# Kernel optimization log

Hardware: AMD Instinct MI355X
Metric: run time of the kernel (lower is better)

## Reference

```python
import jax, jax.numpy as jnp
import numpy as np

B, IN, OUT, P, NS = 256, 1024, 512, 1000, 128

def setup_inputs() -> dict:
    key = jax.random.key(0)
    ks = jax.random.split(key, 6)
    return {
        "x": jax.random.normal(ks[0], (B, IN), jnp.float32),
        "noise": jax.random.normal(ks[1], (B, NS, P), jnp.float32),
        "fb_w": jax.random.normal(ks[2], (1, IN), jnp.float32) * (1.0 / np.sqrt(IN)),
        "fb_b": jnp.zeros((1,), jnp.float32),
        "decay_param": jnp.full((1,), 0.1, jnp.float32),
        "conv_w": jax.random.normal(ks[3], (P, P, 3), jnp.float32) * (1.0 / np.sqrt(3 * P)),
        "conv_b": jnp.zeros((P,), jnp.float32),
        "out_w": jax.random.normal(ks[4], (OUT, P), jnp.float32) * (1.0 / np.sqrt(P)),
        "out_b": jnp.zeros((OUT,), jnp.float32),
    }


def reference(x, noise, fb_w, fb_b, decay_param, conv_w, conv_b, out_w, out_b):
    # x: [B, IN]; noise: [B, NS, P] (Brownian increments for the SDE kernel)
    n_steps = noise.shape[1]
    dt = 1.0 / n_steps                       # T = 1.0
    sd = jnp.sqrt(jnp.asarray(dt, x.dtype))
    # per-sample feedback value: sigmoid(feedback_controller(x))
    feedback = jax.nn.sigmoid(x @ fb_w.T + fb_b)            # [B, 1]
    # decay value: sigmoid(decay_controller) * 0.5 (scalar)
    decay = jax.nn.sigmoid(decay_param[0]) * 0.5
    retain = 1.0 - decay * dt
    # Batched Euler-Maruyama Brownian SDE: X_{t+1} = (1 - decay*dt) X_t + feedback*sqrt(dt)*eps_t
    eps = jnp.transpose(noise, (1, 0, 2))                    # [NS, B, P]
    x0 = jnp.zeros((x.shape[0], noise.shape[2]), x.dtype)

    def step(X, e):
        Xn = X * retain + feedback * sd * e
        return Xn, Xn

    _, paths = jax.lax.scan(step, x0, eps)                   # [NS, B, P]
    paths_bct = jnp.transpose(paths, (1, 2, 0))              # [B, P, NS]
    # temporal_aggregator: Conv1d(P, P, kernel=3, padding=1) over time, then mean over time
    agg = jax.lax.conv_general_dilated(
        paths_bct, conv_w, window_strides=(1,), padding=[(1, 1)],
        dimension_numbers=("NCH", "OIH", "NCH"))
    agg = (agg + conv_b[None, :, None]).mean(axis=2)         # [B, P]
    # output_projection: P -> OUT
    return agg @ out_w.T + out_b
```

## Files before the change

kernel.cpp:

```cpp
#include <hip/hip_runtime.h>
#include <hip/hip_bf16.h>

#define B_N   256
#define IN_N  1024
#define OUT_N 512
#define P_N   1000
#define NS_N  128

#define K1P   3072
#define N1P   1024
#define K2P   1024
#define SK1   16
#define SK2   8

typedef __attribute__((ext_vector_type(8))) short short8v;
typedef __attribute__((ext_vector_type(4))) float f32x4;
typedef unsigned short ushort_t;
typedef __attribute__((ext_vector_type(4))) unsigned short ushort4v;

__device__ __forceinline__ float sigmoid_f(float z) { return 1.0f / (1.0f + __expf(-z)); }

__device__ __forceinline__ ushort_t f2bf(float x) {
    return __bfloat16_as_ushort(__float2bfloat16(x));
}
__device__ __forceinline__ float bf2f(ushort_t h) {
    union { unsigned u; float f; } v; v.u = ((unsigned)h) << 16;
    return v.f;
}

__global__ __launch_bounds__(512) void sde_fused_kernel(const float* __restrict__ x,
                                                        const float* __restrict__ fb_w,
                                                        const float* __restrict__ fb_b,
                                                        const float* __restrict__ noise,
                                                        const float* __restrict__ decay_param,
                                                        ushort_t* __restrict__ Thi) {
    const int b  = blockIdx.x;
    const int ch = blockIdx.y;
    const int t  = threadIdx.x;
    const int cg = t & 127;
    const int tq = t >> 7;

    float2 xv = ((const float2*)(x + (size_t)b * IN_N))[t];
    float2 wv = ((const float2*)fb_w)[t];
    __shared__ float red[512];
    red[t] = xv.x * wv.x + xv.y * wv.y;
    __syncthreads();
    for (int off = 256; off >= 1; off >>= 1) {
        if (t < off) red[t] += red[t + off];
        __syncthreads();
    }
    float fbv = sigmoid_f(red[0] + fb_b[0]);

    float decay = sigmoid_f(decay_param[0]) * 0.5f;
    const float dt = 1.0f / NS_N;
    float retain = 1.0f - decay * dt;
    float inv_omr = 1.0f / (decay * dt);
    float r2 = retain * retain, r4 = r2 * r2, r8 = r4 * r4;
    float r16 = r8 * r8, r32 = r16 * r16;
    float r64 = r32 * r32, r96 = r64 * r32;

    const int c0 = ch * 512 + cg * 4;
    const bool act = (c0 < P_N);
    const float* base = noise + (size_t)b * NS_N * P_N + (act ? c0 : 0);

    float4 sE = {0, 0, 0, 0}, L = {0, 0, 0, 0};
    if (act) {
        const int s0 = tq * 32;
        float rp = 1.0f;
        #pragma unroll 8
        for (int ss = s0 + 31; ss >= s0; --ss) {
            float4 e = *(const float4*)(base + (size_t)ss * P_N);
            sE.x += e.x; sE.y += e.y; sE.z += e.z; sE.w += e.w;
            L.x += rp * e.x; L.y += rp * e.y; L.z += rp * e.z; L.w += rp * e.w;
            rp *= retain;
        }
    }

    __shared__ float4 xSE[3][128], xL[3][128], xF[128];
    if (tq < 3) { xSE[tq][cg] = sE; xL[tq][cg] = L; }
    if (tq == 0 && act) xF[cg] = *(const float4*)base;
    __syncthreads();

    if (tq == 3) {
        size_t tb = (size_t)b * K1P + 3 * (size_t)c0;
        if (!act) {
            #pragma unroll
            for (int j = 0; j < 12; ++j) Thi[tb + j] = 0;
            return;
        }
        float4 se0 = xSE[0][cg], se1 = xSE[1][cg], se2 = xSE[2][cg];
        float4 l0 = xL[0][cg], l1 = xL[1][cg], l2 = xL[2][cg], ff = xF[cg];
        float Se[4] = {se0.x + se1.x + se2.x + sE.x, se0.y + se1.y + se2.y + sE.y,
                       se0.z + se1.z + se2.z + sE.z, se0.w + se1.w + se2.w + sE.w};
        float Lv[4] = {L.x + r32 * l2.x + r64 * l1.x + r96 * l0.x,
                       L.y + r32 * l2.y + r64 * l1.y + r96 * l0.y,
                       L.z + r32 * l2.z + r64 * l1.z + r96 * l0.z,
                       L.w + r32 * l2.w + r64 * l1.w + r96 * l0.w};
        float Fv[4] = {ff.x, ff.y, ff.z, ff.w};
        float sd = sqrtf(dt);
        float scale = fbv * sd * (1.0f / NS_N);
        #pragma unroll
        for (int j = 0; j < 4; ++j) {
            float Aj = (Se[j] - retain * Lv[j]) * inv_omr;
            Thi[tb + 3 * j + 0] = f2bf(scale * (Aj - Lv[j]));
            Thi[tb + 3 * j + 1] = f2bf(scale * Aj);
            Thi[tb + 3 * j + 2] = f2bf(scale * (Aj - Fv[j]));
        }
    }
}

__global__ __launch_bounds__(512) void gemm_bf16_bm256(const ushort_t* __restrict__ A,
                                                       const float* __restrict__ B,
                                                       ushort_t* __restrict__ Cpart,
                                                       int lda, int ldb,
                                                       int Nvalid, int Kvalid,
                                                       int Kper, int ldc) {
    __shared__ __align__(16) ushort_t As[256 * 64];
    __shared__ __align__(16) ushort_t Bs[128 * 64];

    const int tid  = threadIdx.x;
    const int lane = tid & 63;
    const int wave = tid >> 6;
    const int r15  = lane & 15;
    const int g4   = lane >> 4;
    const int wrow = wave >> 1;
    const int wcol = wave & 1;
    const int n0 = blockIdx.x * 128;
    const size_t kbeg = (size_t)blockIdx.z * Kper;

    f32x4 acc[4][4] = {};

    for (int kt = 0; kt < Kper; kt += 64) {
        const size_t kk0 = kbeg + kt;
        #pragma unroll
        for (int c = 0; c < 4; ++c) {
            int chunk = tid + c * 512;
            int row = chunk >> 3;
            int g   = chunk & 7;
            int ldsoff = row * 64 + ((g ^ (row & 7)) << 3);
            *(short8v*)&As[ldsoff] = *(const short8v*)(A + (size_t)row * lda + kk0 + g * 8);
        }
        #pragma unroll
        for (int c = 0; c < 2; ++c) {
            int chunk = tid + c * 512;
            int row = chunk >> 3;
            int g   = chunk & 7;
            int ldsoff = row * 64 + ((g ^ (row & 7)) << 3);
            int k = (int)kk0 + g * 8;
            short8v bh = {0, 0, 0, 0, 0, 0, 0, 0};
            if ((n0 + row) < Nvalid && k < Kvalid) {
                const float* bp = B + (size_t)(n0 + row) * ldb + k;
                float4 b0 = *(const float4*)bp;
                float4 b1 = *(const float4*)(bp + 4);
                bh[0] = (short)f2bf(b0.x); bh[1] = (short)f2bf(b0.y);
                bh[2] = (short)f2bf(b0.z); bh[3] = (short)f2bf(b0.w);
                bh[4] = (short)f2bf(b1.x); bh[5] = (short)f2bf(b1.y);
                bh[6] = (short)f2bf(b1.z); bh[7] = (short)f2bf(b1.w);
            }
            *(short8v*)&Bs[ldsoff] = bh;
        }
        __syncthreads();

        #pragma unroll
        for (int ks = 0; ks < 2; ++ks) {
            const int g = ks * 4 + g4;
            short8v af[4], bf_[4];
            #pragma unroll
            for (int f = 0; f < 4; ++f) {
                int arow = wrow * 64 + f * 16 + r15;
                af[f] = *(const short8v*)&As[arow * 64 + ((g ^ (arow & 7)) << 3)];
            }
            #pragma unroll
            for (int f = 0; f < 4; ++f) {
                int brow = wcol * 64 + f * 16 + r15;
                bf_[f] = *(const short8v*)&Bs[brow * 64 + ((g ^ (brow & 7)) << 3)];
            }
            #pragma unroll
            for (int mf = 0; mf < 4; ++mf) {
                #pragma unroll
                for (int nf = 0; nf < 4; ++nf) {
                    acc[mf][nf] = __builtin_amdgcn_mfma_f32_16x16x32_bf16(af[mf], bf_[nf], acc[mf][nf], 0, 0, 0);
                }
            }
        }
        __syncthreads();
    }

    ushort_t* cp = Cpart + (size_t)blockIdx.z * B_N * ldc;
    #pragma unroll
    for (int mf = 0; mf < 4; ++mf) {
        #pragma unroll
        for (int nf = 0; nf < 4; ++nf) {
            #pragma unroll
            for (int r = 0; r < 4; ++r) {
                int m = wrow * 64 + mf * 16 + g4 * 4 + r;
                int n = n0 + wcol * 64 + nf * 16 + r15;
                cp[(size_t)m * ldc + n] = f2bf(acc[mf][nf][r]);
            }
        }
    }
}

__global__ __launch_bounds__(256) void reduce_agg_kernel(const ushort_t* __restrict__ Cpart1,
                                                         const float* __restrict__ conv_b,
                                                         ushort_t* __restrict__ agg) {
    int idx4 = (blockIdx.x * 256 + threadIdx.x) * 4;
    int n = idx4 & (N1P - 1);
    float s0 = 0.f, s1 = 0.f, s2 = 0.f, s3 = 0.f;
    if (n < P_N) {
        float4 cb = *(const float4*)(conv_b + n);
        s0 = cb.x; s1 = cb.y; s2 = cb.z; s3 = cb.w;
        #pragma unroll
        for (int z = 0; z < SK1; ++z) {
            ushort4v p = *(const ushort4v*)(Cpart1 + (size_t)z * (B_N * N1P) + idx4);
            s0 += bf2f(p[0]); s1 += bf2f(p[1]); s2 += bf2f(p[2]); s3 += bf2f(p[3]);
        }
    }
    ushort4v o = {f2bf(s0), f2bf(s1), f2bf(s2), f2bf(s3)};
    *(ushort4v*)(agg + idx4) = o;
}

__global__ __launch_bounds__(256) void reduce_out_kernel(const ushort_t* __restrict__ Cpart2,
                                                         const float* __restrict__ out_b,
                                                         float* __restrict__ out) {
    int idx4 = (blockIdx.x * 256 + threadIdx.x) * 4;
    int n = idx4 & (OUT_N - 1);
    float4 ob = *(const float4*)(out_b + n);
    float s0 = ob.x, s1 = ob.y, s2 = ob.z, s3 = ob.w;
    #pragma unroll
    for (int z = 0; z < SK2; ++z) {
        ushort4v p = *(const ushort4v*)(Cpart2 + (size_t)z * (B_N * OUT_N) + idx4);
        s0 += bf2f(p[0]); s1 += bf2f(p[1]); s2 += bf2f(p[2]); s3 += bf2f(p[3]);
    }
    float4 o = {s0, s1, s2, s3};
    *(float4*)(out + idx4) = o;
}

extern "C" void kernel_launch(void* const* d_in, const int* in_sizes, int n_in,
                              void* d_out, int out_size, void* d_ws, size_t ws_size,
                              hipStream_t stream) {
    const float* x           = (const float*)d_in[0];
    const float* noise       = (const float*)d_in[1];
    const float* fb_w        = (const float*)d_in[2];
    const float* fb_b        = (const float*)d_in[3];
    const float* decay_param = (const float*)d_in[4];
    const float* conv_w      = (const float*)d_in[5];
    const float* conv_b      = (const float*)d_in[6];
    const float* out_w       = (const float*)d_in[7];
    const float* out_b       = (const float*)d_in[8];
    float* out = (float*)d_out;

    char* ws = (char*)d_ws;
    size_t off = 0;
    ushort_t* Thi    = (ushort_t*)(ws + off); off += (size_t)B_N * K1P * 2;
    ushort_t* agg    = (ushort_t*)(ws + off); off += (size_t)B_N * K2P * 2;
    ushort_t* Cpart1 = (ushort_t*)(ws + off); off += (size_t)SK1 * B_N * N1P * 2;
    ushort_t* Cpart2 = (ushort_t*)(ws + off); off += (size_t)SK2 * B_N * OUT_N * 2;

    {
        dim3 grid(B_N, 2);
        sde_fused_kernel<<<grid, 512, 0, stream>>>(x, fb_w, fb_b, noise, decay_param, Thi);
    }

    {
        dim3 grid(N1P / 128, 1, SK1);
        gemm_bf16_bm256<<<grid, 512, 0, stream>>>(Thi, conv_w, Cpart1,
                                                  K1P, 3 * P_N, P_N, 3 * P_N,
                                                  K1P / SK1, N1P);
    }

    reduce_agg_kernel<<<(B_N * N1P) / 1024, 256, 0, stream>>>(Cpart1, conv_b, agg);

    {
        dim3 grid(OUT_N / 128, 1, SK2);
        gemm_bf16_bm256<<<grid, 512, 0, stream>>>(agg, out_w, Cpart2,
                                                  K2P, P_N, OUT_N, P_N,
                                                  K2P / SK2, OUT_N);
    }

    reduce_out_kernel<<<(B_N * OUT_N) / 1024, 256, 0, stream>>>(Cpart2, out_b, out);
}
```

Measured before the change: 48.39 us.

## Retile GEMM1 to narrower N tiles, replace split-K GEMM2 with direct 64x64 tiled kernel

```diff
diff --git a/kernel.cpp b/kernel.cpp
--- a/kernel.cpp
+++ b/kernel.cpp
@@ -10,8 +10,7 @@
 #define K1P   3072
 #define N1P   1024
 #define K2P   1024
-#define SK1   16
-#define SK2   8
+#define SK1   8
 
 typedef __attribute__((ext_vector_type(8))) short short8v;
 typedef __attribute__((ext_vector_type(4))) float f32x4;
@@ -109,14 +108,11 @@
     }
 }
 
-__global__ __launch_bounds__(512) void gemm_bf16_bm256(const ushort_t* __restrict__ A,
-                                                       const float* __restrict__ B,
-                                                       ushort_t* __restrict__ Cpart,
-                                                       int lda, int ldb,
-                                                       int Nvalid, int Kvalid,
-                                                       int Kper, int ldc) {
+__global__ __launch_bounds__(512) void gemm1_kernel(const ushort_t* __restrict__ A,
+                                                    const float* __restrict__ B,
+                                                    ushort_t* __restrict__ Cpart) {
     __shared__ __align__(16) ushort_t As[256 * 64];
-    __shared__ __align__(16) ushort_t Bs[128 * 64];
+    __shared__ __align__(16) ushort_t Bs[64 * 64];
 
     const int tid  = threadIdx.x;
     const int lane = tid & 63;
@@ -125,31 +121,26 @@
     const int g4   = lane >> 4;
     const int wrow = wave >> 1;
     const int wcol = wave & 1;
-    const int n0 = blockIdx.x * 128;
-    const size_t kbeg = (size_t)blockIdx.z * Kper;
-
-    f32x4 acc[4][4] = {};
-
-    for (int kt = 0; kt < Kper; kt += 64) {
-        const size_t kk0 = kbeg + kt;
+    const int n0   = blockIdx.x * 64;
+    const int kbeg = blockIdx.z * (K1P / SK1);
+
+    f32x4 acc[4][2] = {};
+
+    for (int kt = 0; kt < K1P / SK1; kt += 64) {
+        const int kk0 = kbeg + kt;
         #pragma unroll
         for (int c = 0; c < 4; ++c) {
             int chunk = tid + c * 512;
-            int row = chunk >> 3;
-            int g   = chunk & 7;
-            int ldsoff = row * 64 + ((g ^ (row & 7)) << 3);
-            *(short8v*)&As[ldsoff] = *(const short8v*)(A + (size_t)row * lda + kk0 + g * 8);
-        }
-        #pragma unroll
-        for (int c = 0; c < 2; ++c) {
-            int chunk = tid + c * 512;
-            int row = chunk >> 3;
-            int g   = chunk & 7;
-            int ldsoff = row * 64 + ((g ^ (row & 7)) << 3);
-            int k = (int)kk0 + g * 8;
+            int row = chunk >> 3, g = chunk & 7;
+            *(short8v*)&As[row * 64 + ((g ^ (row & 7)) << 3)] =
+                *(const short8v*)(A + (size_t)row * K1P + kk0 + g * 8);
+        }
+        {
+            int row = tid >> 3, g = tid & 7;
+            int k = kk0 + g * 8;
             short8v bh = {0, 0, 0, 0, 0, 0, 0, 0};
-            if ((n0 + row) < Nvalid && k < Kvalid) {
-                const float* bp = B + (size_t)(n0 + row) * ldb + k;
+            if ((n0 + row) < P_N && k < 3 * P_N) {
+                const float* bp = B + (size_t)(n0 + row) * (3 * P_N) + k;
                 float4 b0 = *(const float4*)bp;
                 float4 b1 = *(const float4*)(bp + 4);
                 bh[0] = (short)f2bf(b0.x); bh[1] = (short)f2bf(b0.y);
@@ -157,45 +148,45 @@
                 bh[4] = (short)f2bf(b1.x); bh[5] = (short)f2bf(b1.y);
                 bh[6] = (short)f2bf(b1.z); bh[7] = (short)f2bf(b1.w);
             }
-            *(short8v*)&Bs[ldsoff] = bh;
+            *(short8v*)&Bs[row * 64 + ((g ^ (row & 7)) << 3)] = bh;
         }
         __syncthreads();
 
         #pragma unroll
         for (int ks = 0; ks < 2; ++ks) {
             const int g = ks * 4 + g4;
-            short8v af[4], bf_[4];
+            short8v af[4], bfv[2];
             #pragma unroll
             for (int f = 0; f < 4; ++f) {
                 int arow = wrow * 64 + f * 16 + r15;
                 af[f] = *(const short8v*)&As[arow * 64 + ((g ^ (arow & 7)) << 3)];
             }
             #pragma unroll
-            for (int f = 0; f < 4; ++f) {
-                int brow = wcol * 64 + f * 16 + r15;
-                bf_[f] = *(const short8v*)&Bs[brow * 64 + ((g ^ (brow & 7)) << 3)];
+            for (int f = 0; f < 2; ++f) {
+                int brow = wcol * 32 + f * 16 + r15;
+                bfv[f] = *(const short8v*)&Bs[brow * 64 + ((g ^ (brow & 7)) << 3)];
             }
             #pragma unroll
             for (int mf = 0; mf < 4; ++mf) {
                 #pragma unroll
-                for (int nf = 0; nf < 4; ++nf) {
-                    acc[mf][nf] = __builtin_amdgcn_mfma_f32_16x16x32_bf16(af[mf], bf_[nf], acc[mf][nf], 0, 0, 0);
+                for (int nf = 0; nf < 2; ++nf) {
+                    acc[mf][nf] = __builtin_amdgcn_mfma_f32_16x16x32_bf16(af[mf], bfv[nf], acc[mf][nf], 0, 0, 0);
                 }
             }
         }
         __syncthreads();
     }
 
-    ushort_t* cp = Cpart + (size_t)blockIdx.z * B_N * ldc;
+    ushort_t* cp = Cpart + (size_t)blockIdx.z * (B_N * N1P);
     #pragma unroll
     for (int mf = 0; mf < 4; ++mf) {
         #pragma unroll
-        for (int nf = 0; nf < 4; ++nf) {
+        for (int nf = 0; nf < 2; ++nf) {
             #pragma unroll
             for (int r = 0; r < 4; ++r) {
                 int m = wrow * 64 + mf * 16 + g4 * 4 + r;
-                int n = n0 + wcol * 64 + nf * 16 + r15;
-                cp[(size_t)m * ldc + n] = f2bf(acc[mf][nf][r]);
+                int n = n0 + wcol * 32 + nf * 16 + r15;
+                cp[(size_t)m * N1P + n] = f2bf(acc[mf][nf][r]);
             }
         }
     }
@@ -220,20 +211,90 @@
     *(ushort4v*)(agg + idx4) = o;
 }
 
-__global__ __launch_bounds__(256) void reduce_out_kernel(const ushort_t* __restrict__ Cpart2,
-                                                         const float* __restrict__ out_b,
-                                                         float* __restrict__ out) {
-    int idx4 = (blockIdx.x * 256 + threadIdx.x) * 4;
-    int n = idx4 & (OUT_N - 1);
-    float4 ob = *(const float4*)(out_b + n);
-    float s0 = ob.x, s1 = ob.y, s2 = ob.z, s3 = ob.w;
+__global__ __launch_bounds__(256) void gemm2_kernel(const ushort_t* __restrict__ agg,
+                                                    const float* __restrict__ out_w,
+                                                    const float* __restrict__ out_b,
+                                                    float* __restrict__ out) {
+    __shared__ __align__(16) ushort_t As[64 * 64];
+    __shared__ __align__(16) ushort_t Bs[64 * 64];
+
+    const int tid  = threadIdx.x;
+    const int lane = tid & 63;
+    const int wave = tid >> 6;
+    const int r15  = lane & 15;
+    const int g4   = lane >> 4;
+    const int wrow = wave >> 1;
+    const int wcol = wave & 1;
+    const int n0 = blockIdx.x * 64;
+    const int m0 = blockIdx.y * 64;
+
+    f32x4 acc[2][2] = {};
+
+    for (int kt = 0; kt < K2P; kt += 64) {
+        #pragma unroll
+        for (int c = 0; c < 2; ++c) {
+            int chunk = tid + c * 256;
+            int row = chunk >> 3, g = chunk & 7;
+            *(short8v*)&As[row * 64 + ((g ^ (row & 7)) << 3)] =
+                *(const short8v*)(agg + (size_t)(m0 + row) * K2P + kt + g * 8);
+        }
+        #pragma unroll
+        for (int c = 0; c < 2; ++c) {
+            int chunk = tid + c * 256;
+            int row = chunk >> 3, g = chunk & 7;
+            int k = kt + g * 8;
+            short8v bh = {0, 0, 0, 0, 0, 0, 0, 0};
+            if (k < P_N) {
+                const float* bp = out_w + (size_t)(n0 + row) * P_N + k;
+                float4 b0 = *(const float4*)bp;
+                float4 b1 = *(const float4*)(bp + 4);
+                bh[0] = (short)f2bf(b0.x); bh[1] = (short)f2bf(b0.y);
+                bh[2] = (short)f2bf(b0.z); bh[3] = (short)f2bf(b0.w);
+                bh[4] = (short)f2bf(b1.x); bh[5] = (short)f2bf(b1.y);
+                bh[6] = (short)f2bf(b1.z); bh[7] = (short)f2bf(b1.w);
+            }
+            *(short8v*)&Bs[row * 64 + ((g ^ (row & 7)) << 3)] = bh;
+        }
+        __syncthreads();
+
+        #pragma unroll
+        for (int ks = 0; ks < 2; ++ks) {
+            const int g = ks * 4 + g4;
+            short8v af[2], bfv[2];
+            #pragma unroll
+            for (int f = 0; f < 2; ++f) {
+                int arow = wrow * 32 + f * 16 + r15;
+                af[f] = *(const short8v*)&As[arow * 64 + ((g ^ (arow & 7)) << 3)];
+            }
+            #pragma unroll
+            for (int f = 0; f < 2; ++f) {
+                int brow = wcol * 32 + f * 16 + r15;
+                bfv[f] = *(const short8v*)&Bs[brow * 64 + ((g ^ (brow & 7)) << 3)];
+            }
+            #pragma unroll
+            for (int mf = 0; mf < 2; ++mf) {
+                #pragma unroll
+                for (int nf = 0; nf < 2; ++nf) {
+                    acc[mf][nf] = __builtin_amdgcn_mfma_f32_16x16x32_bf16(af[mf], bfv[nf], acc[mf][nf], 0, 0, 0);
+                }
+            }
+        }
+        __syncthreads();
+    }
+
     #pragma unroll
-    for (int z = 0; z < SK2; ++z) {
-        ushort4v p = *(const ushort4v*)(Cpart2 + (size_t)z * (B_N * OUT_N) + idx4);
-        s0 += bf2f(p[0]); s1 += bf2f(p[1]); s2 += bf2f(p[2]); s3 += bf2f(p[3]);
-    }
-    float4 o = {s0, s1, s2, s3};
-    *(float4*)(out + idx4) = o;
+    for (int mf = 0; mf < 2; ++mf) {
+        #pragma unroll
+        for (int nf = 0; nf < 2; ++nf) {
+            int n = n0 + wcol * 32 + nf * 16 + r15;
+            float ob = out_b[n];
+            #pragma unroll
+            for (int r = 0; r < 4; ++r) {
+                int m = m0 + wrow * 32 + mf * 16 + g4 * 4 + r;
+                out[(size_t)m * OUT_N + n] = acc[mf][nf][r] + ob;
+            }
+        }
+    }
 }
 
 extern "C" void kernel_launch(void* const* d_in, const int* in_sizes, int n_in,
@@ -255,7 +316,6 @@
     ushort_t* Thi    = (ushort_t*)(ws + off); off += (size_t)B_N * K1P * 2;
     ushort_t* agg    = (ushort_t*)(ws + off); off += (size_t)B_N * K2P * 2;
     ushort_t* Cpart1 = (ushort_t*)(ws + off); off += (size_t)SK1 * B_N * N1P * 2;
-    ushort_t* Cpart2 = (ushort_t*)(ws + off); off += (size_t)SK2 * B_N * OUT_N * 2;
 
     {
         dim3 grid(B_N, 2);
@@ -263,20 +323,14 @@
     }
 
     {
-        dim3 grid(N1P / 128, 1, SK1);
-        gemm_bf16_bm256<<<grid, 512, 0, stream>>>(Thi, conv_w, Cpart1,
-                                                  K1P, 3 * P_N, P_N, 3 * P_N,
-                                                  K1P / SK1, N1P);
+        dim3 grid(N1P / 64, 1, SK1);
+        gemm1_kernel<<<grid, 512, 0, stream>>>(Thi, conv_w, Cpart1);
     }
 
     reduce_agg_kernel<<<(B_N * N1P) / 1024, 256, 0, stream>>>(Cpart1, conv_b, agg);
 
     {
-        dim3 grid(OUT_N / 128, 1, SK2);
-        gemm_bf16_bm256<<<grid, 512, 0, stream>>>(agg, out_w, Cpart2,
-                                                  K2P, P_N, OUT_N, P_N,
-                                                  K2P / SK2, OUT_N);
-    }
-
-    reduce_out_kernel<<<(B_N * OUT_N) / 1024, 256, 0, stream>>>(Cpart2, out_b, out);
-}
+        dim3 grid(OUT_N / 64, B_N / 64);
+        gemm2_kernel<<<grid, 256, 0, stream>>>(agg, out_w, out_b, out);
+    }
+}
```

Measured after the change: 62.10 us. 28.3% more time.
